# Optimization experiments

Measured on AMD Instinct MI355X. Metric: run time of the kernel, lower is better.

The kernel has to match this reference:

```python
import jax, jax.numpy as jnp
import numpy as np

B, S, D, H = 4, 1024, 1024, 16
HD = D // H


def setup_inputs() -> dict:
    key = jax.random.key(0)
    ks = jax.random.split(key, 12)
    s = 1.0 / np.sqrt(D)
    inp = {
        'q': jax.random.normal(ks[0], (B, S, D), jnp.float32),
        'k': jax.random.normal(ks[1], (B, S, D), jnp.float32),
        'v': jax.random.normal(ks[2], (B, S, D), jnp.float32),
        'mask': jnp.broadcast_to(jnp.tril(jnp.ones((S, S), jnp.int32)), (B, S, S)),
        'Wq': jax.random.uniform(ks[3], (D, D), jnp.float32, -s, s),
        'bq': jax.random.uniform(ks[4], (D,), jnp.float32, -s, s),
        'Wk': jax.random.uniform(ks[5], (D, D), jnp.float32, -s, s),
        'bk': jax.random.uniform(ks[6], (D,), jnp.float32, -s, s),
        'Wv': jax.random.uniform(ks[7], (D, D), jnp.float32, -s, s),
        'bv': jax.random.uniform(ks[8], (D,), jnp.float32, -s, s),
        'Wo': jax.random.uniform(ks[9], (D, D), jnp.float32, -s, s),
        'bo': jax.random.uniform(ks[10], (D,), jnp.float32, -s, s),
    }
    return inp


def _split_heads(x):
    # [B,S,D] -> [B,H,S,HD]
    b, s, d = x.shape
    return x.reshape(b, s, H, HD).transpose(0, 2, 1, 3)


def reference(q, k, v, mask, Wq, bq, Wk, bk, Wv, bv, Wo, bo):
    # Linear projections (torch Linear: x @ W.T + b) followed by relu
    qh = jax.nn.relu(q @ Wq.T + bq)
    kh = jax.nn.relu(k @ Wk.T + bk)
    vh = jax.nn.relu(v @ Wv.T + bv)
    qh, kh, vh = _split_heads(qh), _split_heads(kh), _split_heads(vh)
    scores = jnp.einsum('bhqd,bhkd->bhqk', qh, kh) / jnp.sqrt(jnp.float32(HD))
    scores = jnp.where(mask[:, None, :, :] == 0, jnp.float32(-1e9), scores)
    attn = jax.nn.softmax(scores, axis=-1)
    y = jnp.einsum('bhqk,bhkd->bhqd', attn, vh)
    y = y.transpose(0, 2, 1, 3).reshape(B, S, D)  # merge heads
    return jax.nn.relu(y @ Wo.T + bo)
```

## Files before the change

kernel.cpp:

```cpp
#include <hip/hip_runtime.h>


using f16    = _Float16;
using f16x4  = __attribute__((ext_vector_type(4))) _Float16;
using f16x8  = __attribute__((ext_vector_type(8))) _Float16;
using f32x4  = __attribute__((ext_vector_type(4))) float;
using f32x16 = __attribute__((ext_vector_type(16))) float;

static constexpr int S = 1024, Dm = 1024, NH = 16, HD = 64;

#if __has_builtin(__builtin_amdgcn_mfma_f32_32x32x16_f16)
#define USE_G32 1
#define MFMA32(ACC, A_, B_) \
    (ACC) = __builtin_amdgcn_mfma_f32_32x32x16_f16((A_), (B_), (ACC), 0, 0, 0)
#else
#define USE_G32 0
#endif

#if __has_builtin(__builtin_amdgcn_mfma_f32_16x16x32_f16) && \
    __has_builtin(__builtin_amdgcn_mfma_f32_16x16x16f16)
#define USE_A16 1
#define MFMA16K32(ACC, A_, B_) \
    (ACC) = __builtin_amdgcn_mfma_f32_16x16x32_f16((A_), (B_), (ACC), 0, 0, 0)
#define MFMA16(ACC, A_, B_) \
    (ACC) = __builtin_amdgcn_mfma_f32_16x16x16f16((A_), (B_), (ACC), 0, 0, 0)
#else
#define USE_A16 0
#endif

#define LO4(v) __builtin_shufflevector((v), (v), 0, 1, 2, 3)
#define HI4(v) __builtin_shufflevector((v), (v), 4, 5, 6, 7)

__device__ __forceinline__ f16x4 cvt4(float4 a) {
    f16x4 r; r[0] = (f16)a.x; r[1] = (f16)a.y; r[2] = (f16)a.z; r[3] = (f16)a.w;
    return r;
}

__device__ __forceinline__ int pcol64(int k) {
#if USE_A16
    return ((k >> 3) & 3) * 16 + ((k >> 5) << 3) + (k & 7);
#else
    return ((k >> 2) & 3) * 16 + ((k >> 4) << 2) + (k & 3);
#endif
}

__device__ __forceinline__ int swz(int row, int col) {
    return (col & ~63) | ((((col >> 3) ^ row) & 7) << 3) | (col & 7);
}

__device__ __forceinline__ void store_out(void* out, int mode, int m, int n, float v) {
    if (mode == 2) {
        ((float*)out)[(size_t)m * Dm + n] = v;
    } else {
        const int b_ = m >> 10, s_ = m & 1023, h_ = n >> 6, hd_ = n & 63;
        const size_t idx = (mode == 0)
            ? (((size_t)(b_ * NH + h_) * S + s_) * HD + pcol64(hd_))
            : (((size_t)(b_ * NH + h_) * HD + hd_) * S + s_);
        ((f16*)out)[idx] = (f16)v;
    }
}

#if __has_builtin(__builtin_amdgcn_global_load_lds)
#define HAS_GLL 1
#else
#define HAS_GLL 0
#endif

__device__ __forceinline__ void gll16(const f16* g, f16* l) {
#if HAS_GLL
    __builtin_amdgcn_global_load_lds(
        (const __attribute__((address_space(1))) void*)g,
        (__attribute__((address_space(3))) void*)l, 16, 0, 0);
#else
    *(uint4*)l = *(const uint4*)g;
#endif
}

__global__ __launch_bounds__(256)
void cvt_w(const float* __restrict__ s0, const float* __restrict__ s1,
           const float* __restrict__ s2, f16* __restrict__ dst)
{
    const int z = blockIdx.y;
    const float* src = (z == 0) ? s0 : (z == 1) ? s1 : s2;
    const int e = blockIdx.x * 256 + threadIdx.x;
    const int n = e >> 8;
    const int k = (e & 255) * 4;
    const float4 v = *(const float4*)(src + (size_t)n * Dm + k);
    *(f16x4*)(dst + (size_t)z * Dm * Dm + (size_t)n * Dm + swz(n, k)) = cvt4(v);
}

template <int ADMA>
__device__ __forceinline__ void gemm_core(const void* __restrict__ A,
                                          const f16* __restrict__ Wf,
                                          const float* __restrict__ bias,
                                          void* __restrict__ out, int mode)
{
    const int tid = threadIdx.x;
    const int bm = blockIdx.x, bn = blockIdx.y;
#if USE_G32
    __shared__ alignas(16) f16 As[2][128][64];
    __shared__ alignas(16) f16 Ws[2][128][64];

    const int lane = tid & 63, wave = tid >> 6;
    const int l31 = lane & 31, kh = lane >> 5;
    const int wm = wave & 1, wn = wave >> 1;

    const int drow = lane >> 3;
    const int dcol = (lane & 7) * 8;
    const f16* Wsrc = Wf + (size_t)(bn * 128) * Dm + dcol;
    const f16* Asrc = (const f16*)A + (size_t)(bm * 128) * Dm + dcol;

    auto dma = [&](int k0, int cur) {
#pragma unroll
        for (int i = 0; i < 4; ++i) {
            const int r = (i * 4 + wave) * 8 + drow;
            gll16(Wsrc + (size_t)r * Dm + k0, &Ws[cur][r][dcol]);
        }
        if (ADMA) {
#pragma unroll
            for (int i = 0; i < 4; ++i) {
                const int r = (i * 4 + wave) * 8 + drow;
                gll16(Asrc + (size_t)r * Dm + k0, &As[cur][r][dcol]);
            }
        }
    };

    const int ar = tid >> 1;
    const int ah = tid & 1;
    const float* Af = (const float*)A + (size_t)(bm * 128 + ar) * Dm + ah * 16;

    float4 pa[4];
    auto prefA = [&](int k0, int h) {
#pragma unroll
        for (int j = 0; j < 4; ++j)
            pa[j] = *(const float4*)(Af + k0 + h * 32 + j * 4);
    };
    auto stageA = [&](int cur, int h) {
#pragma unroll
        for (int j2 = 0; j2 < 2; ++j2) {
            f16x8 v;
            const float4 a0 = pa[j2 * 2], a1 = pa[j2 * 2 + 1];
            v[0] = (f16)a0.x; v[1] = (f16)a0.y; v[2] = (f16)a0.z; v[3] = (f16)a0.w;
            v[4] = (f16)a1.x; v[5] = (f16)a1.y; v[6] = (f16)a1.z; v[7] = (f16)a1.w;
            const int slot = (h * 4 + ah * 2 + j2) ^ (ar & 7);
            *(f16x8*)&As[cur][ar][slot * 8] = v;
        }
    };

    f32x16 acc[2][2] = {};

    auto kslice = [&](int cur, int s) {
        const int slot = ((s * 2 + kh) ^ (l31 & 7)) * 8;
        const f16x8 af0 = *(const f16x8*)&As[cur][wm * 64 + l31][slot];
        const f16x8 af1 = *(const f16x8*)&As[cur][wm * 64 + 32 + l31][slot];
        const f16x8 bf0 = *(const f16x8*)&Ws[cur][wn * 64 + l31][slot];
        const f16x8 bf1 = *(const f16x8*)&Ws[cur][wn * 64 + 32 + l31][slot];
        MFMA32(acc[0][0], af0, bf0);
        MFMA32(acc[0][1], af0, bf1);
        MFMA32(acc[1][0], af1, bf0);
        MFMA32(acc[1][1], af1, bf1);
    };

    constexpr int NIT = Dm / 64;
    dma(0, 0);
    if (!ADMA) { prefA(0, 0); stageA(0, 0); prefA(0, 1); stageA(0, 1); }
    for (int it = 0; it < NIT; ++it) {
        const int cur = it & 1;
        __syncthreads();
        const bool more = (it < NIT - 1);
        if (more) dma((it + 1) * 64, cur ^ 1);
        if (!ADMA && more) prefA((it + 1) * 64, 0);
        kslice(cur, 0);
        kslice(cur, 1);
        if (!ADMA && more) { stageA(cur ^ 1, 0); prefA((it + 1) * 64, 1); }
        kslice(cur, 2);
        if (!ADMA && more) stageA(cur ^ 1, 1);
        kslice(cur, 3);
    }

#pragma unroll
    for (int g2 = 0; g2 < 2; ++g2) {
        const int col = bn * 128 + wn * 64 + g2 * 32 + l31;
        const float bb = bias[col];
#pragma unroll
        for (int g = 0; g < 2; ++g)
#pragma unroll
            for (int blk = 0; blk < 4; ++blk) {
                const int row0 = bm * 128 + wm * 64 + g * 32 + 8 * blk + 4 * kh;
                if (mode == 1) {
                    const int b_ = row0 >> 10, s_ = row0 & 1023;
                    const int h_ = col >> 6, hd_ = col & 63;
                    f16x4 vv;
#pragma unroll
                    for (int r = 0; r < 4; ++r)
                        vv[r] = (f16)fmaxf(acc[g][g2][blk * 4 + r] + bb, 0.0f);
                    *(f16x4*)&((f16*)out)[((size_t)(b_ * NH + h_) * HD + hd_) * S + s_] = vv;
                } else {
#pragma unroll
                    for (int r = 0; r < 4; ++r)
                        store_out(out, mode, row0 + r, col,
                                  fmaxf(acc[g][g2][blk * 4 + r] + bb, 0.0f));
                }
            }
    }
#else
    for (int i = tid; i < 128 * 128; i += 256) {
        const int m = bm * 128 + (i >> 7);
        const int n = bn * 128 + (i & 127);
        float acc = 0.0f;
        for (int k2 = 0; k2 < Dm; ++k2) {
            const float a = ADMA ? (float)((const f16*)A)[(size_t)m * Dm + swz(m, k2)]
                                 : ((const float*)A)[(size_t)m * Dm + k2];
            acc = fmaf(a, (float)Wf[(size_t)n * Dm + swz(n, k2)], acc);
        }
        store_out(out, mode, m, n, fmaxf(acc + bias[n], 0.0f));
    }
#endif
}

__global__ __launch_bounds__(256)
void gemm_qkv(const float* __restrict__ q, const float* __restrict__ k,
              const float* __restrict__ v, const f16* __restrict__ wqkv,
              const float* __restrict__ bq, const float* __restrict__ bk,
              const float* __restrict__ bv,
              f16* __restrict__ qh, f16* __restrict__ kh, f16* __restrict__ vt)
{
    const int z = blockIdx.z;
    const float* A = (z == 0) ? q : (z == 1) ? k : v;
    const float* B = (z == 0) ? bq : (z == 1) ? bk : bv;
    f16* O = (z == 0) ? qh : (z == 1) ? kh : vt;
    gemm_core<0>(A, wqkv + (size_t)z * Dm * Dm, B, O, (z == 2) ? 1 : 0);
}

__global__ __launch_bounds__(256)
void gemm_out(const f16* __restrict__ y, const f16* __restrict__ wo,
              const float* __restrict__ bo, float* __restrict__ out)
{
    gemm_core<1>(y, wo, bo, out, 2);
}

__global__ __launch_bounds__(256)
void attn_fwd(const f16* __restrict__ qh, const f16* __restrict__ kh,
              const f16* __restrict__ vt, f16* __restrict__ y)
{
    const int bz = blockIdx.x;
    const int qt = bz & 15;
    const int h  = (bz >> 4) & 15;
    const int b  = bz >> 8;
    const size_t head = (size_t)(b * NH + h) * S * HD;

#if USE_A16
    __shared__ alignas(16) f16 Ks[2][64][72];
    __shared__ alignas(16) f16 Vs[2][64][72];

    const int tid  = threadIdx.x;
    const int wave = tid >> 6;
    const int lane = tid & 63;
    const int l15  = lane & 15;
    const int quad = lane >> 4;
    const int sr   = tid >> 2;
    const int sc   = (tid & 3) * 16;

    const f16* Qrow = qh + head + (size_t)(qt * 64 + wave * 16 + l15) * HD;
    const f16* Kp   = kh + head;
    const f16* Vp   = vt + head;

    f16x8 aq[2];
    {
        const uint4 q0 = *(const uint4*)(Qrow + quad * 16);
        const uint4 q1 = *(const uint4*)(Qrow + quad * 16 + 8);
        aq[0] = *(f16x8*)&q0;
        aq[1] = *(f16x8*)&q1;
    }

    const int qg = qt * 64 + wave * 16 + l15;
    float m_i = -1e30f, l_i = 0.0f;
    f32x4 acc_o[4] = {};

    uint4 pk[2], pv[2];
    auto pref = [&](int kt) {
        const f16* Kr = Kp + (size_t)(kt * 64 + sr) * HD + sc;
        pk[0] = *(const uint4*)Kr;
        pk[1] = *(const uint4*)(Kr + 8);
        const f16* Vr = Vp + (size_t)sr * S + kt * 64 + sc;
        pv[0] = *(const uint4*)Vr;
        pv[1] = *(const uint4*)(Vr + 8);
    };

    pref(0);
    for (int kt = 0; kt <= qt; ++kt) {
        const int cur = kt & 1;
        *(uint4*)&Ks[cur][sr][sc]     = pk[0];
        *(uint4*)&Ks[cur][sr][sc + 8] = pk[1];
        {
            const int sb = (sc >> 4) * 4;
            *(f16x4*)&Vs[cur][sr][0 * 16 + sb] = *(f16x4*)((f16*)&pv[0]);
            *(f16x4*)&Vs[cur][sr][1 * 16 + sb] = *(f16x4*)((f16*)&pv[0] + 4);
            *(f16x4*)&Vs[cur][sr][2 * 16 + sb] = *(f16x4*)((f16*)&pv[1]);
            *(f16x4*)&Vs[cur][sr][3 * 16 + sb] = *(f16x4*)((f16*)&pv[1] + 4);
        }
        __syncthreads();
        if (kt < qt) pref(kt + 1);

        f32x4 accs[4] = {};
#pragma unroll
        for (int t = 0; t < 4; ++t) {
            const f16x8 k8a = *(const f16x8*)&Ks[cur][t * 16 + l15][quad * 16];
            const f16x8 k8b = *(const f16x8*)&Ks[cur][t * 16 + l15][quad * 16 + 8];
            MFMA16K32(accs[t], k8a, aq[0]);
            MFMA16K32(accs[t], k8b, aq[1]);
        }

        const int key0 = kt * 64 + quad * 4;
#pragma unroll
        for (int t = 0; t < 4; ++t)
#pragma unroll
            for (int r = 0; r < 4; ++r) {
                float sv = accs[t][r] * 0.125f;
                if (key0 + t * 16 + r > qg) sv = -1e9f;
                accs[t][r] = sv;
            }

        float mx = accs[0][0];
#pragma unroll
        for (int t = 0; t < 4; ++t)
#pragma unroll
            for (int r = 0; r < 4; ++r) mx = fmaxf(mx, accs[t][r]);
        mx = fmaxf(mx, __shfl_xor(mx, 16, 64));
        mx = fmaxf(mx, __shfl_xor(mx, 32, 64));
        const float mnew = fmaxf(m_i, mx);
        float sm = 0.0f;
#pragma unroll
        for (int t = 0; t < 4; ++t)
#pragma unroll
            for (int r = 0; r < 4; ++r) {
                const float e = __expf(accs[t][r] - mnew);
                accs[t][r] = e;
                sm += e;
            }
        sm += __shfl_xor(sm, 16, 64);
        sm += __shfl_xor(sm, 32, 64);
        const float alpha = __expf(m_i - mnew);
        l_i = l_i * alpha + sm;
        m_i = mnew;

        f16x4 ap[4];
#pragma unroll
        for (int c = 0; c < 4; ++c) {
            f16x4 v;
#pragma unroll
            for (int j = 0; j < 4; ++j) v[j] = (f16)accs[c][j];
            ap[c] = v;
        }

        float ar[4];
#pragma unroll
        for (int r = 0; r < 4; ++r) ar[r] = __shfl(alpha, quad * 4 + r, 64);
#pragma unroll
        for (int t2 = 0; t2 < 4; ++t2)
#pragma unroll
            for (int r = 0; r < 4; ++r) acc_o[t2][r] *= ar[r];
#pragma unroll
        for (int t2 = 0; t2 < 4; ++t2) {
            const f16x8 v8a = *(const f16x8*)&Vs[cur][t2 * 16 + l15][quad * 16];
            const f16x8 v8b = *(const f16x8*)&Vs[cur][t2 * 16 + l15][quad * 16 + 8];
            MFMA16(acc_o[t2], ap[0], LO4(v8a));
            MFMA16(acc_o[t2], ap[1], HI4(v8a));
            MFMA16(acc_o[t2], ap[2], LO4(v8b));
            MFMA16(acc_o[t2], ap[3], HI4(v8b));
        }
    }

    float lr[4];
#pragma unroll
    for (int r = 0; r < 4; ++r) lr[r] = __shfl(l_i, quad * 4 + r, 64);
#pragma unroll
    for (int t2 = 0; t2 < 4; ++t2)
#pragma unroll
        for (int r = 0; r < 4; ++r) {
            const int srow = qt * 64 + wave * 16 + quad * 4 + r;
            const int dcol = h * 64 + t2 * 16 + l15;
            y[((size_t)b * S + srow) * Dm + swz(srow, dcol)] =
                (f16)(acc_o[t2][r] / lr[r]);
        }
#else
    const int tid = threadIdx.x;
    if (tid < 64) {
        const int q = qt * 64 + tid;
        const f16* Qr = qh + head + (size_t)q * HD;
        float qv[64];
        for (int d = 0; d < 64; ++d) qv[d] = (float)Qr[pcol64(d)];
        float mx = -1e30f;
        for (int key = 0; key <= q; ++key) {
            const f16* Kr = kh + head + (size_t)key * HD;
            float s = 0.0f;
            for (int d = 0; d < 64; ++d) s = fmaf(qv[d], (float)Kr[pcol64(d)], s);
            mx = fmaxf(mx, s * 0.125f);
        }
        float o[64];
        for (int d = 0; d < 64; ++d) o[d] = 0.0f;
        float l = 0.0f;
        for (int key = 0; key <= q; ++key) {
            const f16* Kr = kh + head + (size_t)key * HD;
            float s = 0.0f;
            for (int d = 0; d < 64; ++d) s = fmaf(qv[d], (float)Kr[pcol64(d)], s);
            const float p = __expf(s * 0.125f - mx);
            l += p;
            for (int d = 0; d < 64; ++d)
                o[d] = fmaf(p, (float)vt[head + (size_t)d * S + key], o[d]);
        }
        for (int d = 0; d < 64; ++d)
            y[((size_t)b * S + q) * Dm + swz(q, h * 64 + d)] = (f16)(o[d] / l);
    }
#endif
}

extern "C" void kernel_launch(void* const* d_in, const int* in_sizes, int n_in,
                              void* d_out, int out_size, void* d_ws, size_t ws_size,
                              hipStream_t stream)
{
    f16* ws = (f16*)d_ws;
    const size_t SEG = (size_t)4 * 1024 * 1024;
    f16* qh   = ws;
    f16* kh   = ws + SEG;
    f16* vt   = ws + 2 * SEG;
    f16* wqkv = ws + 3 * SEG;
    f16* y    = ws + 3 * SEG;
    f16* wo   = ws;

    cvt_w<<<dim3(1024, 3), 256, 0, stream>>>(
        (const float*)d_in[4], (const float*)d_in[6], (const float*)d_in[8], wqkv);
    gemm_qkv<<<dim3(32, 8, 3), 256, 0, stream>>>(
        (const float*)d_in[0], (const float*)d_in[1], (const float*)d_in[2],
        wqkv,
        (const float*)d_in[5], (const float*)d_in[7], (const float*)d_in[9],
        qh, kh, vt);
    attn_fwd<<<dim3(4 * NH * (S / 64)), 256, 0, stream>>>(qh, kh, vt, y);
    cvt_w<<<dim3(1024, 1), 256, 0, stream>>>(
        (const float*)d_in[10], nullptr, nullptr, wo);
    gemm_out<<<dim3(32, 8), 256, 0, stream>>>(
        y, wo, (const float*)d_in[11], (float*)d_out);
}
```

Baseline: 274.6 us.

## Triple-buffer GEMM with BK=32 tiles and explicit vmcnt-based pipelining

Restructures the shared GEMM core from a double-buffered BK=64 loop into a triple-buffered BK=32 pipeline. Loads are issued two iterations ahead, and a plain __syncthreads is replaced by explicit s_waitcnt counters and a raw barrier. The LDS swizzle and the weight pre-swizzle are changed to match 32-wide rows. Occupancy is raised via launch_bounds(256,3) and the smaller LDS footprint. This aims to hide global-load latency better, at the cost of twice as many barriers and hand-tuned vmcnt values that must exactly match the number of outstanding loads.

```diff
diff --git a/kernel.cpp b/kernel.cpp
--- a/kernel.cpp
+++ b/kernel.cpp
@@ -45,7 +45,7 @@
 }
 
 __device__ __forceinline__ int swz(int row, int col) {
-    return (col & ~63) | ((((col >> 3) ^ row) & 7) << 3) | (col & 7);
+    return (col & ~31) | ((((col >> 3) ^ (row >> 1)) & 3) << 3) | (col & 7);
 }
 
 __device__ __forceinline__ void store_out(void* out, int mode, int m, int n, float v) {
@@ -98,84 +98,94 @@
     const int tid = threadIdx.x;
     const int bm = blockIdx.x, bn = blockIdx.y;
 #if USE_G32
-    __shared__ alignas(16) f16 As[2][128][64];
-    __shared__ alignas(16) f16 Ws[2][128][64];
+    __shared__ alignas(16) f16 As[3][128][32];
+    __shared__ alignas(16) f16 Ws[3][128][32];
 
     const int lane = tid & 63, wave = tid >> 6;
     const int l31 = lane & 31, kh = lane >> 5;
     const int wm = wave & 1, wn = wave >> 1;
 
-    const int drow = lane >> 3;
-    const int dcol = (lane & 7) * 8;
-    const f16* Wsrc = Wf + (size_t)(bn * 128) * Dm + dcol;
-    const f16* Asrc = (const f16*)A + (size_t)(bm * 128) * Dm + dcol;
-
-    auto dma = [&](int k0, int cur) {
-#pragma unroll
-        for (int i = 0; i < 4; ++i) {
-            const int r = (i * 4 + wave) * 8 + drow;
-            gll16(Wsrc + (size_t)r * Dm + k0, &Ws[cur][r][dcol]);
-        }
+    const int drow = wave * 16 + (lane >> 2);
+    const int dcol = (lane & 3) * 8;
+    const f16* Wsrc = Wf + (size_t)(bn * 128 + drow) * Dm + dcol;
+    const f16* Asrc = (const f16*)A + (size_t)(bm * 128 + drow) * Dm + dcol;
+
+    auto dma = [&](int k0, int buf) {
+        gll16(Wsrc + k0, &Ws[buf][drow][dcol]);
+        gll16(Wsrc + k0 + (size_t)64 * Dm, &Ws[buf][64 + drow][dcol]);
         if (ADMA) {
-#pragma unroll
-            for (int i = 0; i < 4; ++i) {
-                const int r = (i * 4 + wave) * 8 + drow;
-                gll16(Asrc + (size_t)r * Dm + k0, &As[cur][r][dcol]);
-            }
-        }
-    };
-
-    const int ar = tid >> 1;
-    const int ah = tid & 1;
+            gll16(Asrc + k0, &As[buf][drow][dcol]);
+            gll16(Asrc + k0 + (size_t)64 * Dm, &As[buf][64 + drow][dcol]);
+        }
+    };
+
+    const int ar = tid >> 1, ah = tid & 1;
     const float* Af = (const float*)A + (size_t)(bm * 128 + ar) * Dm + ah * 16;
 
-    float4 pa[4];
-    auto prefA = [&](int k0, int h) {
-#pragma unroll
-        for (int j = 0; j < 4; ++j)
-            pa[j] = *(const float4*)(Af + k0 + h * 32 + j * 4);
-    };
-    auto stageA = [&](int cur, int h) {
+    auto prefA = [&](int k0, float4 (&pa)[4]) {
+#pragma unroll
+        for (int j = 0; j < 4; ++j) pa[j] = *(const float4*)(Af + k0 + j * 4);
+    };
+    auto stageA = [&](int buf, const float4 (&pa)[4]) {
 #pragma unroll
         for (int j2 = 0; j2 < 2; ++j2) {
             f16x8 v;
             const float4 a0 = pa[j2 * 2], a1 = pa[j2 * 2 + 1];
             v[0] = (f16)a0.x; v[1] = (f16)a0.y; v[2] = (f16)a0.z; v[3] = (f16)a0.w;
             v[4] = (f16)a1.x; v[5] = (f16)a1.y; v[6] = (f16)a1.z; v[7] = (f16)a1.w;
-            const int slot = (h * 4 + ah * 2 + j2) ^ (ar & 7);
-            *(f16x8*)&As[cur][ar][slot * 8] = v;
+            const int phys = ((ah * 2 + j2) ^ ((ar >> 1) & 3)) & 3;
+            *(f16x8*)&As[buf][ar][phys * 8] = v;
         }
     };
 
     f32x16 acc[2][2] = {};
 
-    auto kslice = [&](int cur, int s) {
-        const int slot = ((s * 2 + kh) ^ (l31 & 7)) * 8;
-        const f16x8 af0 = *(const f16x8*)&As[cur][wm * 64 + l31][slot];
-        const f16x8 af1 = *(const f16x8*)&As[cur][wm * 64 + 32 + l31][slot];
-        const f16x8 bf0 = *(const f16x8*)&Ws[cur][wn * 64 + l31][slot];
-        const f16x8 bf1 = *(const f16x8*)&Ws[cur][wn * 64 + 32 + l31][slot];
+    auto kslice = [&](int buf, int s) {
+        const int sl = s * 2 + kh;
+        const int rA0 = wm * 64 + l31,  rA1 = wm * 64 + 32 + l31;
+        const int rB0 = wn * 64 + l31,  rB1 = wn * 64 + 32 + l31;
+        const f16x8 af0 = *(const f16x8*)&As[buf][rA0][((sl ^ ((rA0 >> 1) & 3)) & 3) * 8];
+        const f16x8 af1 = *(const f16x8*)&As[buf][rA1][((sl ^ ((rA1 >> 1) & 3)) & 3) * 8];
+        const f16x8 bf0 = *(const f16x8*)&Ws[buf][rB0][((sl ^ ((rB0 >> 1) & 3)) & 3) * 8];
+        const f16x8 bf1 = *(const f16x8*)&Ws[buf][rB1][((sl ^ ((rB1 >> 1) & 3)) & 3) * 8];
         MFMA32(acc[0][0], af0, bf0);
         MFMA32(acc[0][1], af0, bf1);
         MFMA32(acc[1][0], af1, bf0);
         MFMA32(acc[1][1], af1, bf1);
     };
 
-    constexpr int NIT = Dm / 64;
+    constexpr int NIT = Dm / 32;
+    float4 paA[4], paB[4];
+
+    if (!ADMA) prefA(0, paA);
     dma(0, 0);
-    if (!ADMA) { prefA(0, 0); stageA(0, 0); prefA(0, 1); stageA(0, 1); }
-    for (int it = 0; it < NIT; ++it) {
-        const int cur = it & 1;
-        __syncthreads();
-        const bool more = (it < NIT - 1);
-        if (more) dma((it + 1) * 64, cur ^ 1);
-        if (!ADMA && more) prefA((it + 1) * 64, 0);
-        kslice(cur, 0);
-        kslice(cur, 1);
-        if (!ADMA && more) { stageA(cur ^ 1, 0); prefA((it + 1) * 64, 1); }
-        kslice(cur, 2);
-        if (!ADMA && more) stageA(cur ^ 1, 1);
-        kslice(cur, 3);
+    if (!ADMA) prefA(32, paB);
+    dma(32, 1);
+    if (!ADMA) stageA(0, paA);
+
+    auto iter = [&](int t, float4 (&pnew)[4], const float4 (&pold)[4]) {
+        if (t < NIT - 1) {
+            if (ADMA) asm volatile("s_waitcnt vmcnt(4)" ::: "memory");
+            else      asm volatile("s_waitcnt vmcnt(6)" ::: "memory");
+        } else {
+            asm volatile("s_waitcnt vmcnt(0)" ::: "memory");
+        }
+        asm volatile("s_waitcnt lgkmcnt(0)" ::: "memory");
+        __builtin_amdgcn_s_barrier();
+        __builtin_amdgcn_sched_barrier(0);
+        const int cb = t % 3;
+        if (t + 2 < NIT) {
+            if (!ADMA) prefA((t + 2) * 32, pnew);
+            dma((t + 2) * 32, (t + 2) % 3);
+        }
+        kslice(cb, 0);
+        if (!ADMA && t + 1 < NIT) stageA((t + 1) % 3, pold);
+        kslice(cb, 1);
+    };
+
+    for (int t = 0; t < NIT; t += 2) {
+        iter(t, paA, paB);
+        iter(t + 1, paB, paA);
     }
 
 #pragma unroll
@@ -218,7 +228,7 @@
 #endif
 }
 
-__global__ __launch_bounds__(256)
+__global__ __launch_bounds__(256, 3)
 void gemm_qkv(const float* __restrict__ q, const float* __restrict__ k,
               const float* __restrict__ v, const f16* __restrict__ wqkv,
               const float* __restrict__ bq, const float* __restrict__ bk,
@@ -232,7 +242,7 @@
     gemm_core<0>(A, wqkv + (size_t)z * Dm * Dm, B, O, (z == 2) ? 1 : 0);
 }
 
-__global__ __launch_bounds__(256)
+__global__ __launch_bounds__(256, 3)
 void gemm_out(const f16* __restrict__ y, const f16* __restrict__ wo,
               const float* __restrict__ bo, float* __restrict__ out)
 {
```

Measured after the change: 259.2 us. 1.06x faster.

## Restructure projection GEMMs: DMA fp32 activations to LDS, K32 tiles, smaller output tiles

Applied to the files above, without the earlier changes.

The QKV GEMM now loads fp32 activations straight into LDS with global_load_lds and converts them to f16 when fragments are read. This replaces the register prefetch, convert and store staging. Both GEMMs move to 32-wide K slices with a matching 4-slot swizzle and set occupancy hints in launch_bounds. The output GEMM shrinks to 64x64 tiles, so the grid has four times as many blocks and fills the CUs better. The cost is twice the LDS traffic for fp32 A, repeated conversion by waves that share the same A fragments, and more loop iterations and barriers.

```diff
diff --git a/kernel.cpp b/kernel.cpp
--- a/kernel.cpp
+++ b/kernel.cpp
@@ -45,19 +45,15 @@
 }
 
 __device__ __forceinline__ int swz(int row, int col) {
-    return (col & ~63) | ((((col >> 3) ^ row) & 7) << 3) | (col & 7);
+    return (col & ~31) | ((((col >> 3) ^ (row >> 1)) & 3) << 3) | (col & 7);
 }
 
 __device__ __forceinline__ void store_out(void* out, int mode, int m, int n, float v) {
-    if (mode == 2) {
-        ((float*)out)[(size_t)m * Dm + n] = v;
-    } else {
-        const int b_ = m >> 10, s_ = m & 1023, h_ = n >> 6, hd_ = n & 63;
-        const size_t idx = (mode == 0)
-            ? (((size_t)(b_ * NH + h_) * S + s_) * HD + pcol64(hd_))
-            : (((size_t)(b_ * NH + h_) * HD + hd_) * S + s_);
-        ((f16*)out)[idx] = (f16)v;
-    }
+    const int b_ = m >> 10, s_ = m & 1023, h_ = n >> 6, hd_ = n & 63;
+    const size_t idx = (mode == 0)
+        ? (((size_t)(b_ * NH + h_) * S + s_) * HD + pcol64(hd_))
+        : (((size_t)(b_ * NH + h_) * HD + hd_) * S + s_);
+    ((f16*)out)[idx] = (f16)v;
 }
 
 #if __has_builtin(__builtin_amdgcn_global_load_lds)
@@ -66,7 +62,7 @@
 #define HAS_GLL 0
 #endif
 
-__device__ __forceinline__ void gll16(const f16* g, f16* l) {
+__device__ __forceinline__ void gll16(const void* g, void* l) {
 #if HAS_GLL
     __builtin_amdgcn_global_load_lds(
         (const __attribute__((address_space(1))) void*)g,
@@ -89,136 +85,7 @@
     *(f16x4*)(dst + (size_t)z * Dm * Dm + (size_t)n * Dm + swz(n, k)) = cvt4(v);
 }
 
-template <int ADMA>
-__device__ __forceinline__ void gemm_core(const void* __restrict__ A,
-                                          const f16* __restrict__ Wf,
-                                          const float* __restrict__ bias,
-                                          void* __restrict__ out, int mode)
-{
-    const int tid = threadIdx.x;
-    const int bm = blockIdx.x, bn = blockIdx.y;
-#if USE_G32
-    __shared__ alignas(16) f16 As[2][128][64];
-    __shared__ alignas(16) f16 Ws[2][128][64];
-
-    const int lane = tid & 63, wave = tid >> 6;
-    const int l31 = lane & 31, kh = lane >> 5;
-    const int wm = wave & 1, wn = wave >> 1;
-
-    const int drow = lane >> 3;
-    const int dcol = (lane & 7) * 8;
-    const f16* Wsrc = Wf + (size_t)(bn * 128) * Dm + dcol;
-    const f16* Asrc = (const f16*)A + (size_t)(bm * 128) * Dm + dcol;
-
-    auto dma = [&](int k0, int cur) {
-#pragma unroll
-        for (int i = 0; i < 4; ++i) {
-            const int r = (i * 4 + wave) * 8 + drow;
-            gll16(Wsrc + (size_t)r * Dm + k0, &Ws[cur][r][dcol]);
-        }
-        if (ADMA) {
-#pragma unroll
-            for (int i = 0; i < 4; ++i) {
-                const int r = (i * 4 + wave) * 8 + drow;
-                gll16(Asrc + (size_t)r * Dm + k0, &As[cur][r][dcol]);
-            }
-        }
-    };
-
-    const int ar = tid >> 1;
-    const int ah = tid & 1;
-    const float* Af = (const float*)A + (size_t)(bm * 128 + ar) * Dm + ah * 16;
-
-    float4 pa[4];
-    auto prefA = [&](int k0, int h) {
-#pragma unroll
-        for (int j = 0; j < 4; ++j)
-            pa[j] = *(const float4*)(Af + k0 + h * 32 + j * 4);
-    };
-    auto stageA = [&](int cur, int h) {
-#pragma unroll
-        for (int j2 = 0; j2 < 2; ++j2) {
-            f16x8 v;
-            const float4 a0 = pa[j2 * 2], a1 = pa[j2 * 2 + 1];
-            v[0] = (f16)a0.x; v[1] = (f16)a0.y; v[2] = (f16)a0.z; v[3] = (f16)a0.w;
-            v[4] = (f16)a1.x; v[5] = (f16)a1.y; v[6] = (f16)a1.z; v[7] = (f16)a1.w;
-            const int slot = (h * 4 + ah * 2 + j2) ^ (ar & 7);
-            *(f16x8*)&As[cur][ar][slot * 8] = v;
-        }
-    };
-
-    f32x16 acc[2][2] = {};
-
-    auto kslice = [&](int cur, int s) {
-        const int slot = ((s * 2 + kh) ^ (l31 & 7)) * 8;
-        const f16x8 af0 = *(const f16x8*)&As[cur][wm * 64 + l31][slot];
-        const f16x8 af1 = *(const f16x8*)&As[cur][wm * 64 + 32 + l31][slot];
-        const f16x8 bf0 = *(const f16x8*)&Ws[cur][wn * 64 + l31][slot];
-        const f16x8 bf1 = *(const f16x8*)&Ws[cur][wn * 64 + 32 + l31][slot];
-        MFMA32(acc[0][0], af0, bf0);
-        MFMA32(acc[0][1], af0, bf1);
-        MFMA32(acc[1][0], af1, bf0);
-        MFMA32(acc[1][1], af1, bf1);
-    };
-
-    constexpr int NIT = Dm / 64;
-    dma(0, 0);
-    if (!ADMA) { prefA(0, 0); stageA(0, 0); prefA(0, 1); stageA(0, 1); }
-    for (int it = 0; it < NIT; ++it) {
-        const int cur = it & 1;
-        __syncthreads();
-        const bool more = (it < NIT - 1);
-        if (more) dma((it + 1) * 64, cur ^ 1);
-        if (!ADMA && more) prefA((it + 1) * 64, 0);
-        kslice(cur, 0);
-        kslice(cur, 1);
-        if (!ADMA && more) { stageA(cur ^ 1, 0); prefA((it + 1) * 64, 1); }
-        kslice(cur, 2);
-        if (!ADMA && more) stageA(cur ^ 1, 1);
-        kslice(cur, 3);
-    }
-
-#pragma unroll
-    for (int g2 = 0; g2 < 2; ++g2) {
-        const int col = bn * 128 + wn * 64 + g2 * 32 + l31;
-        const float bb = bias[col];
-#pragma unroll
-        for (int g = 0; g < 2; ++g)
-#pragma unroll
-            for (int blk = 0; blk < 4; ++blk) {
-                const int row0 = bm * 128 + wm * 64 + g * 32 + 8 * blk + 4 * kh;
-                if (mode == 1) {
-                    const int b_ = row0 >> 10, s_ = row0 & 1023;
-                    const int h_ = col >> 6, hd_ = col & 63;
-                    f16x4 vv;
-#pragma unroll
-                    for (int r = 0; r < 4; ++r)
-                        vv[r] = (f16)fmaxf(acc[g][g2][blk * 4 + r] + bb, 0.0f);
-                    *(f16x4*)&((f16*)out)[((size_t)(b_ * NH + h_) * HD + hd_) * S + s_] = vv;
-                } else {
-#pragma unroll
-                    for (int r = 0; r < 4; ++r)
-                        store_out(out, mode, row0 + r, col,
-                                  fmaxf(acc[g][g2][blk * 4 + r] + bb, 0.0f));
-                }
-            }
-    }
-#else
-    for (int i = tid; i < 128 * 128; i += 256) {
-        const int m = bm * 128 + (i >> 7);
-        const int n = bn * 128 + (i & 127);
-        float acc = 0.0f;
-        for (int k2 = 0; k2 < Dm; ++k2) {
-            const float a = ADMA ? (float)((const f16*)A)[(size_t)m * Dm + swz(m, k2)]
-                                 : ((const float*)A)[(size_t)m * Dm + k2];
-            acc = fmaf(a, (float)Wf[(size_t)n * Dm + swz(n, k2)], acc);
-        }
-        store_out(out, mode, m, n, fmaxf(acc + bias[n], 0.0f));
-    }
-#endif
-}
-
-__global__ __launch_bounds__(256)
+__global__ __launch_bounds__(256, 3)
 void gemm_qkv(const float* __restrict__ q, const float* __restrict__ k,
               const float* __restrict__ v, const f16* __restrict__ wqkv,
               const float* __restrict__ bq, const float* __restrict__ bk,
@@ -227,16 +94,172 @@
 {
     const int z = blockIdx.z;
     const float* A = (z == 0) ? q : (z == 1) ? k : v;
-    const float* B = (z == 0) ? bq : (z == 1) ? bk : bv;
-    f16* O = (z == 0) ? qh : (z == 1) ? kh : vt;
-    gemm_core<0>(A, wqkv + (size_t)z * Dm * Dm, B, O, (z == 2) ? 1 : 0);
-}
-
-__global__ __launch_bounds__(256)
+    const float* bias = (z == 0) ? bq : (z == 1) ? bk : bv;
+    f16* out = (z == 0) ? qh : (z == 1) ? kh : vt;
+    const int mode = (z == 2) ? 1 : 0;
+    const f16* Wf = wqkv + (size_t)z * Dm * Dm;
+
+    const int tid = threadIdx.x;
+    const int bm = blockIdx.x, bn = blockIdx.y;
+#if USE_G32
+    __shared__ alignas(16) float As[2][128][32];
+    __shared__ alignas(16) f16   Ws[2][128][32];
+
+    const int lane = tid & 63, wave = tid >> 6;
+    const int l31 = lane & 31, kh2 = lane >> 5;
+    const int wm = wave & 1, wn = wave >> 1;
+
+    const int arow = tid >> 3;
+    const int aslotD = tid & 7;
+    const int aslotS = aslotD ^ (arow & 7);
+    const float* Asrc0 = A + (size_t)(bm * 128 + arow) * Dm + aslotS * 4;
+    const int wrow = tid >> 2, wcol = (tid & 3) * 8;
+    const f16* Wsrc0 = Wf + (size_t)(bn * 128 + wrow) * Dm + wcol;
+
+    auto dma = [&](int k0, int buf) {
+#pragma unroll
+        for (int ch = 0; ch < 4; ++ch)
+            gll16(Asrc0 + (size_t)ch * 32 * Dm + k0,
+                  &As[buf][ch * 32 + arow][aslotD * 4]);
+        gll16(Wsrc0 + k0,                    &Ws[buf][wrow][wcol]);
+        gll16(Wsrc0 + (size_t)64 * Dm + k0,  &Ws[buf][64 + wrow][wcol]);
+    };
+
+    auto afrag = [&](int buf, int r, int s) -> f16x8 {
+        const int p = s * 4 + kh2 * 2, r7 = r & 7;
+        const f32x4 lo = *(const f32x4*)&As[buf][r][(p ^ r7) * 4];
+        const f32x4 hi = *(const f32x4*)&As[buf][r][((p + 1) ^ r7) * 4];
+        f16x8 f;
+        f[0] = (f16)lo[0]; f[1] = (f16)lo[1]; f[2] = (f16)lo[2]; f[3] = (f16)lo[3];
+        f[4] = (f16)hi[0]; f[5] = (f16)hi[1]; f[6] = (f16)hi[2]; f[7] = (f16)hi[3];
+        return f;
+    };
+    auto wfrag = [&](int buf, int r, int s) -> f16x8 {
+        const int sl = s * 2 + kh2;
+        return *(const f16x8*)&Ws[buf][r][((sl ^ (r >> 1)) & 3) * 8];
+    };
+
+    f32x16 acc[2][2] = {};
+    auto kslice = [&](int buf, int s) {
+        const f16x8 af0 = afrag(buf, wm * 64 + l31, s);
+        const f16x8 af1 = afrag(buf, wm * 64 + 32 + l31, s);
+        const f16x8 bf0 = wfrag(buf, wn * 64 + l31, s);
+        const f16x8 bf1 = wfrag(buf, wn * 64 + 32 + l31, s);
+        MFMA32(acc[0][0], af0, bf0);
+        MFMA32(acc[0][1], af0, bf1);
+        MFMA32(acc[1][0], af1, bf0);
+        MFMA32(acc[1][1], af1, bf1);
+    };
+
+    constexpr int NIT = Dm / 32;
+    dma(0, 0);
+    for (int t = 0; t < NIT; ++t) {
+        const int cur = t & 1;
+        __syncthreads();
+        if (t + 1 < NIT) dma((t + 1) * 32, cur ^ 1);
+        kslice(cur, 0);
+        kslice(cur, 1);
+    }
+
+#pragma unroll
+    for (int g2 = 0; g2 < 2; ++g2) {
+        const int col = bn * 128 + wn * 64 + g2 * 32 + l31;
+        const float bb = bias[col];
+#pragma unroll
+        for (int g = 0; g < 2; ++g)
+#pragma unroll
+            for (int blk = 0; blk < 4; ++blk) {
+                const int row0 = bm * 128 + wm * 64 + g * 32 + 8 * blk + 4 * kh2;
+                if (mode == 1) {
+                    const int b_ = row0 >> 10, s_ = row0 & 1023;
+                    const int h_ = col >> 6, hd_ = col & 63;
+                    f16x4 vv;
+#pragma unroll
+                    for (int r = 0; r < 4; ++r)
+                        vv[r] = (f16)fmaxf(acc[g][g2][blk * 4 + r] + bb, 0.0f);
+                    *(f16x4*)&out[((size_t)(b_ * NH + h_) * HD + hd_) * S + s_] = vv;
+                } else {
+#pragma unroll
+                    for (int r = 0; r < 4; ++r)
+                        store_out(out, mode, row0 + r, col,
+                                  fmaxf(acc[g][g2][blk * 4 + r] + bb, 0.0f));
+                }
+            }
+    }
+#else
+    for (int i = tid; i < 128 * 128; i += 256) {
+        const int m = bm * 128 + (i >> 7);
+        const int n = bn * 128 + (i & 127);
+        float acc = 0.0f;
+        for (int k2 = 0; k2 < Dm; ++k2)
+            acc = fmaf(A[(size_t)m * Dm + k2], (float)Wf[(size_t)n * Dm + swz(n, k2)], acc);
+        store_out(out, mode, m, n, fmaxf(acc + bias[n], 0.0f));
+    }
+#endif
+}
+
+__global__ __launch_bounds__(256, 4)
 void gemm_out(const f16* __restrict__ y, const f16* __restrict__ wo,
               const float* __restrict__ bo, float* __restrict__ out)
 {
-    gemm_core<1>(y, wo, bo, out, 2);
+    const int tid = threadIdx.x;
+    const int bm = blockIdx.x, bn = blockIdx.y;
+#if USE_G32
+    __shared__ alignas(16) f16 As[2][64][32];
+    __shared__ alignas(16) f16 Ws[2][64][32];
+
+    const int lane = tid & 63, wave = tid >> 6;
+    const int l31 = lane & 31, kh2 = lane >> 5;
+    const int wm = wave & 1, wn = wave >> 1;
+
+    const int drow = tid >> 2, dcol = (tid & 3) * 8;
+    const f16* Asrc = y  + (size_t)(bm * 64 + drow) * Dm + dcol;
+    const f16* Wsrc = wo + (size_t)(bn * 64 + drow) * Dm + dcol;
+
+    auto dma = [&](int k0, int buf) {
+        gll16(Asrc + k0, &As[buf][drow][dcol]);
+        gll16(Wsrc + k0, &Ws[buf][drow][dcol]);
+    };
+    auto frag = [&](const f16 (&L)[64][32], int r, int s) -> f16x8 {
+        const int sl = s * 2 + kh2;
+        return *(const f16x8*)&L[r][((sl ^ (r >> 1)) & 3) * 8];
+    };
+
+    f32x16 acc = {};
+    constexpr int NIT = Dm / 32;
+    dma(0, 0);
+    for (int t = 0; t < NIT; ++t) {
+        const int cur = t & 1;
+        __syncthreads();
+        if (t + 1 < NIT) dma((t + 1) * 32, cur ^ 1);
+#pragma unroll
+        for (int s = 0; s < 2; ++s) {
+            const f16x8 af = frag(As[cur], wm * 32 + l31, s);
+            const f16x8 bf = frag(Ws[cur], wn * 32 + l31, s);
+            MFMA32(acc, af, bf);
+        }
+    }
+
+    const int col = bn * 64 + wn * 32 + l31;
+    const float bb = bo[col];
+#pragma unroll
+    for (int blk = 0; blk < 4; ++blk) {
+        const int row0 = bm * 64 + wm * 32 + 8 * blk + 4 * kh2;
+#pragma unroll
+        for (int r = 0; r < 4; ++r)
+            out[(size_t)(row0 + r) * Dm + col] = fmaxf(acc[blk * 4 + r] + bb, 0.0f);
+    }
+#else
+    for (int i = tid; i < 64 * 64; i += 256) {
+        const int m = bm * 64 + (i >> 6);
+        const int n = bn * 64 + (i & 63);
+        float acc = 0.0f;
+        for (int k2 = 0; k2 < Dm; ++k2)
+            acc = fmaf((float)y[(size_t)m * Dm + swz(m, k2)],
+                       (float)wo[(size_t)n * Dm + swz(n, k2)], acc);
+        out[(size_t)m * Dm + n] = fmaxf(acc + bo[n], 0.0f);
+    }
+#endif
 }
 
 __global__ __launch_bounds__(256)
@@ -438,6 +461,6 @@
     attn_fwd<<<dim3(4 * NH * (S / 64)), 256, 0, stream>>>(qh, kh, vt, y);
     cvt_w<<<dim3(1024, 1), 256, 0, stream>>>(
         (const float*)d_in[10], nullptr, nullptr, wo);
-    gemm_out<<<dim3(32, 8), 256, 0, stream>>>(
+    gemm_out<<<dim3(64, 16), 256, 0, stream>>>(
         y, wo, (const float*)d_in[11], (float*)d_out);
 }
```

Result: faster. 253.5 us (-7.7%).
